# Performance work log

Measured on AMD Instinct MI355X. Metric: run time of the kernel, lower is better.

Reference implementation:

```python
import jax, jax.numpy as jnp
import numpy as np

B, C_IN, H, W = 4, 1536, 64, 64   # SGI input: cat of three 512-ch encoder maps at 64x64
HID, OUT = 1536, 512
N = H * W


def _grid_edge_index(h, w):
    # 4-connected bidirectional grid, matching SGI.grid_edge_index
    idx = np.arange(h * w).reshape(h, w)
    right = np.stack([idx[:, :-1].ravel(), idx[:, 1:].ravel()])
    down = np.stack([idx[:-1, :].ravel(), idx[1:, :].ravel()])
    ei = np.concatenate([right, down, right[::-1], down[::-1]], axis=1)
    return ei.astype(np.int32)


def setup_inputs() -> dict:
    key = jax.random.key(0)
    ks = jax.random.split(key, 7)
    ei = _grid_edge_index(H, W)
    s = 0.02
    return {
        "x":  jax.random.normal(ks[0], (B, C_IN, H, W), jnp.float32),
        "W1": jax.random.normal(ks[1], (C_IN, HID), jnp.float32) * s,
        "b1": jnp.zeros((HID,), jnp.float32),
        "W2": jax.random.normal(ks[2], (HID, OUT), jnp.float32) * s,
        "b2": jnp.zeros((OUT,), jnp.float32),
        "Wl": jax.random.normal(ks[3], (C_IN, OUT), jnp.float32) * s,
        "bl": jnp.zeros((OUT,), jnp.float32),
        "src": jnp.asarray(ei[0]),
        "dst": jnp.asarray(ei[1]),
    }


def _gcn(h_in, Wt, b, src, dst, inv_sqrt_deg, inv_deg):
    # PyG GCNConv: lin -> symmetric-normalized aggregation (with self loops) -> +bias
    h = h_in @ Wt                                   # [B, N, F]
    norm = inv_sqrt_deg[src] * inv_sqrt_deg[dst]    # [E]
    msgs = h[:, src, :] * norm[None, :, None]       # [B, E, F]
    # self-loop contribution has norm 1/deg_i
    agg = (h * inv_deg[None, :, None]).at[:, dst, :].add(msgs)
    return agg + b


def reference(x, W1, b1, W2, b2, Wl, bl, src, dst):
    Bb, C, Hh, Ww = x.shape
    n = Hh * Ww
    # degree including self loop (graph is symmetric)
    deg = jnp.zeros((n,), x.dtype).at[dst].add(1.0) + 1.0
    inv_sqrt_deg = jax.lax.rsqrt(deg)
    inv_deg = 1.0 / deg

    xt = x.reshape(Bb, C, n).transpose(0, 2, 1)     # [B, N, C]
    identity = xt
    origin = xt @ Wl + bl                           # [B, N, OUT]
    h = jax.nn.relu(_gcn(xt, W1, b1, src, dst, inv_sqrt_deg, inv_deg))
    h = _gcn(h + identity, W2, b2, src, dst, inv_sqrt_deg, inv_deg)
    out = h * origin                                # [B, N, OUT]
    return out.transpose(0, 2, 1).reshape(Bb, out.shape[-1], Hh, Ww)
```

## Files before the change

kernel.cpp:

```cpp
#include <hip/hip_runtime.h>
#include <hip/hip_bf16.h>
#include <stdint.h>


typedef __bf16 bf16;
typedef float f32x4 __attribute__((ext_vector_type(4)));
typedef bf16 bf16x8 __attribute__((ext_vector_type(8)));

#define NB 4
#define NN 4096
#define CIN 1536
#define HIDF 1536
#define OUTF 512

__global__ __launch_bounds__(256) void transpose_cvt(
    const float* __restrict__ in, bf16* __restrict__ out,
    int R, int Cc, long in_bstride, long out_bstride) {
  __shared__ float tile[32][33];
  const float* inb = in + (long)blockIdx.z * in_bstride;
  bf16* outb = out + (long)blockIdx.z * out_bstride;
  const int c0 = blockIdx.x * 32, r0 = blockIdx.y * 32;
  const int tx = threadIdx.x, ty = threadIdx.y;
#pragma unroll
  for (int i = 0; i < 4; i++)
    tile[ty + i * 8][tx] = inb[(long)(r0 + ty + i * 8) * Cc + c0 + tx];
  __syncthreads();
#pragma unroll
  for (int i = 0; i < 4; i++)
    outb[(long)(c0 + ty + i * 8) * R + r0 + tx] = (bf16)tile[tx][ty + i * 8];
}

__device__ __forceinline__ void async_copy16(const void* g, void* l) {
  __builtin_amdgcn_global_load_lds(
      (const __attribute__((address_space(1))) void*)g,
      (__attribute__((address_space(3))) void*)l, 16, 0, 0);
}

template <typename OutT, bool ADD_BIAS>
__global__ __launch_bounds__(256) void gemm_bt(
    const bf16* __restrict__ A, const bf16* __restrict__ Bw,
    OutT* __restrict__ C, const float* __restrict__ bias, int Nf, int K) {
  __shared__ bf16 As[128 * 64];
  __shared__ bf16 Bs[128 * 64];
  const int t = threadIdx.x;
  const int wave = t >> 6, lane = t & 63;
  const int wm = (wave & 1) * 64, wn = (wave >> 1) * 64;
  const int m0 = blockIdx.x * 128;
  const int n0 = blockIdx.y * 128;
  const bf16* Ab = A + (long)blockIdx.z * NN * K + (long)m0 * K;
  const bf16* Bb = Bw + (long)n0 * K;
  OutT* Cb = C + (long)blockIdx.z * NN * Nf;

  const int r = lane >> 3;
  const int c8 = lane & 7;
  const int fchunk = c8 ^ r;

  f32x4 acc[4][4];
#pragma unroll
  for (int i = 0; i < 4; i++)
#pragma unroll
    for (int j = 0; j < 4; j++) acc[i][j] = {0.f, 0.f, 0.f, 0.f};

  const int quad = lane >> 4;
  const int l15 = lane & 15;

  for (int kt = 0; kt < K; kt += 64) {
#pragma unroll
    for (int i = 0; i < 4; i++) {
      const int row = i * 32 + wave * 8;
      async_copy16(Ab + (long)(row + r) * K + kt + fchunk * 8,
                   &As[row * 64]);
      async_copy16(Bb + (long)(row + r) * K + kt + fchunk * 8,
                   &Bs[row * 64]);
    }
    __syncthreads();
#pragma unroll
    for (int kk = 0; kk < 2; kk++) {
      const int q = kk * 4 + quad;
      bf16x8 af[4], bfv[4];
#pragma unroll
      for (int mr = 0; mr < 4; mr++) {
        const int m = wm + mr * 16 + l15;
        af[mr] = *(const bf16x8*)&As[m * 64 + (q ^ (m & 7)) * 8];
      }
#pragma unroll
      for (int nc = 0; nc < 4; nc++) {
        const int n = wn + nc * 16 + l15;
        bfv[nc] = *(const bf16x8*)&Bs[n * 64 + (q ^ (n & 7)) * 8];
      }
#pragma unroll
      for (int mr = 0; mr < 4; mr++)
#pragma unroll
        for (int nc = 0; nc < 4; nc++)
          acc[mr][nc] = __builtin_amdgcn_mfma_f32_16x16x32_bf16(
              af[mr], bfv[nc], acc[mr][nc], 0, 0, 0);
    }
    __syncthreads();
  }

#pragma unroll
  for (int mr = 0; mr < 4; mr++) {
#pragma unroll
    for (int nc = 0; nc < 4; nc++) {
      const int gn = n0 + wn + nc * 16 + l15;
      float bv = 0.f;
      if (ADD_BIAS) bv = bias[gn];
#pragma unroll
      for (int j = 0; j < 4; j++) {
        const int gm = m0 + wm + mr * 16 + quad * 4 + j;
        Cb[(long)gm * Nf + gn] = (OutT)(acc[mr][nc][j] + bv);
      }
    }
  }
}

__device__ __forceinline__ float degree_of(int n) {
  const int x = n & 63, y = n >> 6;
  return 1.0f + (x > 0) + (x < 63) + (y > 0) + (y < 63);
}

__global__ __launch_bounds__(192) void stencil1(
    const bf16* __restrict__ G1, const float* __restrict__ b1, bf16* xt) {
  const int n = blockIdx.x, b = blockIdx.y;
  const int t = threadIdx.x;
  const int gx = n & 63, gy = n >> 6;
  const float degn = degree_of(n);
  const float wself = 1.0f / degn;
  const long base = ((long)b * NN + n) * (long)HIDF + t * 8;

  float acc[8];
  {
    bf16x8 v = *(const bf16x8*)(G1 + base);
#pragma unroll
    for (int i = 0; i < 8; i++) acc[i] = (float)v[i] * wself;
  }
  if (gx > 0) {
    const float w = rsqrtf(degn * degree_of(n - 1));
    bf16x8 u = *(const bf16x8*)(G1 + base - HIDF);
#pragma unroll
    for (int i = 0; i < 8; i++) acc[i] += (float)u[i] * w;
  }
  if (gx < 63) {
    const float w = rsqrtf(degn * degree_of(n + 1));
    bf16x8 u = *(const bf16x8*)(G1 + base + HIDF);
#pragma unroll
    for (int i = 0; i < 8; i++) acc[i] += (float)u[i] * w;
  }
  if (gy > 0) {
    const float w = rsqrtf(degn * degree_of(n - 64));
    bf16x8 u = *(const bf16x8*)(G1 + base - 64L * HIDF);
#pragma unroll
    for (int i = 0; i < 8; i++) acc[i] += (float)u[i] * w;
  }
  if (gy < 63) {
    const float w = rsqrtf(degn * degree_of(n + 64));
    bf16x8 u = *(const bf16x8*)(G1 + base + 64L * HIDF);
#pragma unroll
    for (int i = 0; i < 8; i++) acc[i] += (float)u[i] * w;
  }

  bf16x8 xv = *(const bf16x8*)(xt + base);
  bf16x8 o;
#pragma unroll
  for (int i = 0; i < 8; i++) {
    float h = acc[i] + b1[t * 8 + i];
    h = h > 0.f ? h : 0.f;
    o[i] = (bf16)(h + (float)xv[i]);
  }
  *(bf16x8*)(xt + base) = o;
}

__global__ __launch_bounds__(256) void stencil2(
    const float* __restrict__ G2, const float* __restrict__ Orig,
    const float* __restrict__ b2, float* __restrict__ out) {
  __shared__ float tile[16][513];
  const int n0 = blockIdx.x * 16, b = blockIdx.y;
  const int t = threadIdx.x;
  const int fq = t & 127, nl = t >> 7;
  const int f = fq * 4;
  const f32x4 bv = *(const f32x4*)(b2 + f);
#pragma unroll
  for (int p = 0; p < 8; p++) {
    const int nLoc = p * 2 + nl;
    const int n = n0 + nLoc;
    const int gx = n & 63, gy = n >> 6;
    const float degn = degree_of(n);
    const float ws = 1.0f / degn;
    const long rb = ((long)b * NN + n) * (long)OUTF + f;
    f32x4 g = *(const f32x4*)(G2 + rb);
    f32x4 a;
#pragma unroll
    for (int i = 0; i < 4; i++) a[i] = g[i] * ws;
    if (gx > 0) {
      const float w = rsqrtf(degn * degree_of(n - 1));
      f32x4 u = *(const f32x4*)(G2 + rb - OUTF);
#pragma unroll
      for (int i = 0; i < 4; i++) a[i] += u[i] * w;
    }
    if (gx < 63) {
      const float w = rsqrtf(degn * degree_of(n + 1));
      f32x4 u = *(const f32x4*)(G2 + rb + OUTF);
#pragma unroll
      for (int i = 0; i < 4; i++) a[i] += u[i] * w;
    }
    if (gy > 0) {
      const float w = rsqrtf(degn * degree_of(n - 64));
      f32x4 u = *(const f32x4*)(G2 + rb - 64L * OUTF);
#pragma unroll
      for (int i = 0; i < 4; i++) a[i] += u[i] * w;
    }
    if (gy < 63) {
      const float w = rsqrtf(degn * degree_of(n + 64));
      f32x4 u = *(const f32x4*)(G2 + rb + 64L * OUTF);
#pragma unroll
      for (int i = 0; i < 4; i++) a[i] += u[i] * w;
    }
    f32x4 og = *(const f32x4*)(Orig + rb);
#pragma unroll
    for (int i = 0; i < 4; i++) tile[nLoc][f + i] = (a[i] + bv[i]) * og[i];
  }
  __syncthreads();
  const int nl2 = t & 15, f0 = t >> 4;
#pragma unroll
  for (int q = 0; q < 32; q++) {
    const int ff = q * 16 + f0;
    out[((long)b * OUTF + ff) * (long)NN + n0 + nl2] = tile[nl2][ff];
  }
}

extern "C" void kernel_launch(void* const* d_in, const int* in_sizes, int n_in,
                              void* d_out, int out_size, void* d_ws,
                              size_t ws_size, hipStream_t stream) {
  const float* x = (const float*)d_in[0];
  const float* W1 = (const float*)d_in[1];
  const float* b1 = (const float*)d_in[2];
  const float* W2 = (const float*)d_in[3];
  const float* b2 = (const float*)d_in[4];
  const float* Wl = (const float*)d_in[5];
  const float* bl = (const float*)d_in[6];
  float* out = (float*)d_out;

  uint8_t* ws = (uint8_t*)d_ws;
  size_t off = 0;
  auto alloc = [&](size_t bytes) -> void* {
    void* p = ws + off;
    off += (bytes + 255) & ~(size_t)255;
    return p;
  };
  bf16* xt = (bf16*)alloc((size_t)NB * NN * CIN * 2);
  bf16* g1 = (bf16*)alloc((size_t)NB * NN * HIDF * 2);
  bf16* w1t = (bf16*)alloc((size_t)HIDF * CIN * 2);
  bf16* w2t = (bf16*)alloc((size_t)OUTF * HIDF * 2);
  bf16* wlt = (bf16*)alloc((size_t)OUTF * CIN * 2);
  float* g2 = (float*)alloc((size_t)NB * NN * OUTF * 4);
  float* origin = (float*)alloc((size_t)NB * NN * OUTF * 4);

  const dim3 tb(32, 8);
  transpose_cvt<<<dim3(NN / 32, CIN / 32, NB), tb, 0, stream>>>(
      x, xt, CIN, NN, (long)CIN * NN, (long)NN * CIN);
  transpose_cvt<<<dim3(HIDF / 32, CIN / 32, 1), tb, 0, stream>>>(
      W1, w1t, CIN, HIDF, 0, 0);
  transpose_cvt<<<dim3(OUTF / 32, HIDF / 32, 1), tb, 0, stream>>>(
      W2, w2t, HIDF, OUTF, 0, 0);
  transpose_cvt<<<dim3(OUTF / 32, CIN / 32, 1), tb, 0, stream>>>(
      Wl, wlt, CIN, OUTF, 0, 0);

  gemm_bt<bf16, false><<<dim3(NN / 128, HIDF / 128, NB), 256, 0, stream>>>(
      xt, w1t, g1, nullptr, HIDF, CIN);
  gemm_bt<float, true><<<dim3(NN / 128, OUTF / 128, NB), 256, 0, stream>>>(
      xt, wlt, origin, bl, OUTF, CIN);
  stencil1<<<dim3(NN, NB), 192, 0, stream>>>(g1, b1, xt);
  gemm_bt<float, false><<<dim3(NN / 128, OUTF / 128, NB), 256, 0, stream>>>(
      xt, w2t, g2, nullptr, OUTF, HIDF);
  stencil2<<<dim3(NN / 16, NB), 256, 0, stream>>>(g2, origin, b2, out);
}
```

Measured before the change: 399.4 us.

## Merge transposes and the two input GEMMs into single launches, remap stencil blocks

Folds the four transpose/convert launches into one prep kernel and concatenates W1 and Wl so the first GEMM and the origin GEMM run as one launch over a wider N dimension. Stencil1 now handles 8 nodes per block and reads its bias once, and both stencil kernels permute their block index so that consecutive blocks land on spread-out node ranges. The aim is to cut launch count, tail effects and bias reloads. It adds index arithmetic and may reduce L2 locality for the neighbour reads in the stencils.

```diff
diff --git a/kernel.cpp b/kernel.cpp
--- a/kernel.cpp
+++ b/kernel.cpp
@@ -13,21 +13,50 @@
 #define HIDF 1536
 #define OUTF 512
 
-__global__ __launch_bounds__(256) void transpose_cvt(
-    const float* __restrict__ in, bf16* __restrict__ out,
-    int R, int Cc, long in_bstride, long out_bstride) {
+__device__ __forceinline__ void tcvt(const float* __restrict__ in,
+                                     bf16* __restrict__ out, int R, int Cc,
+                                     int c0, int r0, int t,
+                                     float (*tile)[33]) {
+  const int tx = t & 31, ty = t >> 5;
+#pragma unroll
+  for (int i = 0; i < 4; i++)
+    tile[ty + i * 8][tx] = in[(long)(r0 + ty + i * 8) * Cc + c0 + tx];
+  __syncthreads();
+#pragma unroll
+  for (int i = 0; i < 4; i++)
+    out[(long)(c0 + ty + i * 8) * R + r0 + tx] = (bf16)tile[tx][ty + i * 8];
+}
+
+#define XTILES (NB * (NN / 32) * (CIN / 32))
+#define W1TILES ((CIN / 32) * (HIDF / 32))
+#define W2TILES ((HIDF / 32) * (OUTF / 32))
+#define WLTILES ((CIN / 32) * (OUTF / 32))
+
+__global__ __launch_bounds__(256) void prep(
+    const float* __restrict__ x, const float* __restrict__ W1,
+    const float* __restrict__ W2, const float* __restrict__ Wl,
+    bf16* __restrict__ xt, bf16* __restrict__ w1t, bf16* __restrict__ w2t,
+    bf16* __restrict__ wlt) {
   __shared__ float tile[32][33];
-  const float* inb = in + (long)blockIdx.z * in_bstride;
-  bf16* outb = out + (long)blockIdx.z * out_bstride;
-  const int c0 = blockIdx.x * 32, r0 = blockIdx.y * 32;
-  const int tx = threadIdx.x, ty = threadIdx.y;
-#pragma unroll
-  for (int i = 0; i < 4; i++)
-    tile[ty + i * 8][tx] = inb[(long)(r0 + ty + i * 8) * Cc + c0 + tx];
-  __syncthreads();
-#pragma unroll
-  for (int i = 0; i < 4; i++)
-    outb[(long)(c0 + ty + i * 8) * R + r0 + tx] = (bf16)tile[tx][ty + i * 8];
+  const int b = blockIdx.x, t = threadIdx.x;
+  if (b < XTILES) {
+    const int batch = b / (XTILES / NB), local = b % (XTILES / NB);
+    const int cx = local & 127, ry = local >> 7;
+    tcvt(x + (long)batch * CIN * NN, xt + (long)batch * NN * CIN, CIN, NN,
+         cx * 32, ry * 32, t, tile);
+  } else if (b < XTILES + W1TILES) {
+    const int local = b - XTILES;
+    const int cx = local % 48, ry = local / 48;
+    tcvt(W1, w1t, CIN, HIDF, cx * 32, ry * 32, t, tile);
+  } else if (b < XTILES + W1TILES + W2TILES) {
+    const int local = b - XTILES - W1TILES;
+    const int cx = local % 16, ry = local / 16;
+    tcvt(W2, w2t, HIDF, OUTF, cx * 32, ry * 32, t, tile);
+  } else {
+    const int local = b - XTILES - W1TILES - W2TILES;
+    const int cx = local % 16, ry = local / 16;
+    tcvt(Wl, wlt, CIN, OUTF, cx * 32, ry * 32, t, tile);
+  }
 }
 
 __device__ __forceinline__ void async_copy16(const void* g, void* l) {
@@ -36,82 +65,126 @@
       (__attribute__((address_space(3))) void*)l, 16, 0, 0);
 }
 
-template <typename OutT, bool ADD_BIAS>
-__global__ __launch_bounds__(256) void gemm_bt(
+struct GemmCtx {
+  f32x4 acc[4][4];
+  int wave, lane, wm, wn, quad, l15;
+};
+
+template <int K>
+__device__ __forceinline__ void gemm_kloop(GemmCtx& cx, const bf16* Ab,
+                                           const bf16* Bb, bf16* As,
+                                           bf16* Bs) {
+  const int r = cx.lane >> 3, c8 = cx.lane & 7;
+  const int fchunk = c8 ^ r;
+  for (int kt = 0; kt < K; kt += 64) {
+#pragma unroll
+    for (int i = 0; i < 4; i++) {
+      const int row = i * 32 + cx.wave * 8;
+      async_copy16(Ab + (long)(row + r) * K + kt + fchunk * 8, &As[row * 64]);
+      async_copy16(Bb + (long)(row + r) * K + kt + fchunk * 8, &Bs[row * 64]);
+    }
+    __syncthreads();
+#pragma unroll
+    for (int kk = 0; kk < 2; kk++) {
+      const int q = kk * 4 + cx.quad;
+      bf16x8 af[4], bfv[4];
+#pragma unroll
+      for (int mr = 0; mr < 4; mr++) {
+        const int m = cx.wm + mr * 16 + cx.l15;
+        af[mr] = *(const bf16x8*)&As[m * 64 + (q ^ (m & 7)) * 8];
+      }
+#pragma unroll
+      for (int nc = 0; nc < 4; nc++) {
+        const int n = cx.wn + nc * 16 + cx.l15;
+        bfv[nc] = *(const bf16x8*)&Bs[n * 64 + (q ^ (n & 7)) * 8];
+      }
+#pragma unroll
+      for (int mr = 0; mr < 4; mr++)
+#pragma unroll
+        for (int nc = 0; nc < 4; nc++)
+          cx.acc[mr][nc] = __builtin_amdgcn_mfma_f32_16x16x32_bf16(
+              af[mr], bfv[nc], cx.acc[mr][nc], 0, 0, 0);
+    }
+    __syncthreads();
+  }
+}
+
+__device__ __forceinline__ void gemm_init(GemmCtx& cx, int t) {
+  cx.wave = t >> 6;
+  cx.lane = t & 63;
+  cx.wm = (cx.wave & 1) * 64;
+  cx.wn = (cx.wave >> 1) * 64;
+  cx.quad = cx.lane >> 4;
+  cx.l15 = cx.lane & 15;
+#pragma unroll
+  for (int i = 0; i < 4; i++)
+#pragma unroll
+    for (int j = 0; j < 4; j++) cx.acc[i][j] = {0.f, 0.f, 0.f, 0.f};
+}
+
+__global__ __launch_bounds__(256) void gemm_dual(
     const bf16* __restrict__ A, const bf16* __restrict__ Bw,
-    OutT* __restrict__ C, const float* __restrict__ bias, int Nf, int K) {
+    bf16* __restrict__ G1, float* __restrict__ Orig,
+    const float* __restrict__ bl) {
   __shared__ bf16 As[128 * 64];
   __shared__ bf16 Bs[128 * 64];
-  const int t = threadIdx.x;
-  const int wave = t >> 6, lane = t & 63;
-  const int wm = (wave & 1) * 64, wn = (wave >> 1) * 64;
-  const int m0 = blockIdx.x * 128;
-  const int n0 = blockIdx.y * 128;
-  const bf16* Ab = A + (long)blockIdx.z * NN * K + (long)m0 * K;
-  const bf16* Bb = Bw + (long)n0 * K;
-  OutT* Cb = C + (long)blockIdx.z * NN * Nf;
-
-  const int r = lane >> 3;
-  const int c8 = lane & 7;
-  const int fchunk = c8 ^ r;
-
-  f32x4 acc[4][4];
-#pragma unroll
-  for (int i = 0; i < 4; i++)
-#pragma unroll
-    for (int j = 0; j < 4; j++) acc[i][j] = {0.f, 0.f, 0.f, 0.f};
-
-  const int quad = lane >> 4;
-  const int l15 = lane & 15;
-
-  for (int kt = 0; kt < K; kt += 64) {
-#pragma unroll
-    for (int i = 0; i < 4; i++) {
-      const int row = i * 32 + wave * 8;
-      async_copy16(Ab + (long)(row + r) * K + kt + fchunk * 8,
-                   &As[row * 64]);
-      async_copy16(Bb + (long)(row + r) * K + kt + fchunk * 8,
-                   &Bs[row * 64]);
-    }
-    __syncthreads();
-#pragma unroll
-    for (int kk = 0; kk < 2; kk++) {
-      const int q = kk * 4 + quad;
-      bf16x8 af[4], bfv[4];
-#pragma unroll
-      for (int mr = 0; mr < 4; mr++) {
-        const int m = wm + mr * 16 + l15;
-        af[mr] = *(const bf16x8*)&As[m * 64 + (q ^ (m & 7)) * 8];
-      }
+  GemmCtx cx;
+  gemm_init(cx, threadIdx.x);
+  const int m0 = blockIdx.x * 128, n0 = blockIdx.y * 128, z = blockIdx.z;
+  gemm_kloop<CIN>(cx, A + (long)z * NN * CIN + (long)m0 * CIN,
+                  Bw + (long)n0 * CIN, As, Bs);
+  if (n0 < HIDF) {
+    bf16* Cb = G1 + (long)z * NN * HIDF;
+#pragma unroll
+    for (int mr = 0; mr < 4; mr++)
 #pragma unroll
       for (int nc = 0; nc < 4; nc++) {
-        const int n = wn + nc * 16 + l15;
-        bfv[nc] = *(const bf16x8*)&Bs[n * 64 + (q ^ (n & 7)) * 8];
-      }
-#pragma unroll
-      for (int mr = 0; mr < 4; mr++)
-#pragma unroll
-        for (int nc = 0; nc < 4; nc++)
-          acc[mr][nc] = __builtin_amdgcn_mfma_f32_16x16x32_bf16(
-              af[mr], bfv[nc], acc[mr][nc], 0, 0, 0);
-    }
-    __syncthreads();
-  }
-
-#pragma unroll
-  for (int mr = 0; mr < 4; mr++) {
+        const int gn = n0 + cx.wn + nc * 16 + cx.l15;
+#pragma unroll
+        for (int j = 0; j < 4; j++) {
+          const int gm = m0 + cx.wm + mr * 16 + cx.quad * 4 + j;
+          Cb[(long)gm * HIDF + gn] = (bf16)cx.acc[mr][nc][j];
+        }
+      }
+  } else {
+    float* Cb = Orig + (long)z * NN * OUTF;
+#pragma unroll
+    for (int mr = 0; mr < 4; mr++)
+#pragma unroll
+      for (int nc = 0; nc < 4; nc++) {
+        const int gn = (n0 - HIDF) + cx.wn + nc * 16 + cx.l15;
+        const float bv = bl[gn];
+#pragma unroll
+        for (int j = 0; j < 4; j++) {
+          const int gm = m0 + cx.wm + mr * 16 + cx.quad * 4 + j;
+          Cb[(long)gm * OUTF + gn] = cx.acc[mr][nc][j] + bv;
+        }
+      }
+  }
+}
+
+__global__ __launch_bounds__(256) void gemm_f32(
+    const bf16* __restrict__ A, const bf16* __restrict__ Bw,
+    float* __restrict__ C, int Nf) {
+  __shared__ bf16 As[128 * 64];
+  __shared__ bf16 Bs[128 * 64];
+  GemmCtx cx;
+  gemm_init(cx, threadIdx.x);
+  const int m0 = blockIdx.x * 128, n0 = blockIdx.y * 128, z = blockIdx.z;
+  gemm_kloop<HIDF>(cx, A + (long)z * NN * HIDF + (long)m0 * HIDF,
+                   Bw + (long)n0 * HIDF, As, Bs);
+  float* Cb = C + (long)z * NN * Nf;
+#pragma unroll
+  for (int mr = 0; mr < 4; mr++)
 #pragma unroll
     for (int nc = 0; nc < 4; nc++) {
-      const int gn = n0 + wn + nc * 16 + l15;
-      float bv = 0.f;
-      if (ADD_BIAS) bv = bias[gn];
+      const int gn = n0 + cx.wn + nc * 16 + cx.l15;
 #pragma unroll
       for (int j = 0; j < 4; j++) {
-        const int gm = m0 + wm + mr * 16 + quad * 4 + j;
-        Cb[(long)gm * Nf + gn] = (OutT)(acc[mr][nc][j] + bv);
-      }
-    }
-  }
+        const int gm = m0 + cx.wm + mr * 16 + cx.quad * 4 + j;
+        Cb[(long)gm * Nf + gn] = cx.acc[mr][nc][j];
+      }
+    }
 }
 
 __device__ __forceinline__ float degree_of(int n) {
@@ -121,60 +194,72 @@
 
 __global__ __launch_bounds__(192) void stencil1(
     const bf16* __restrict__ G1, const float* __restrict__ b1, bf16* xt) {
-  const int n = blockIdx.x, b = blockIdx.y;
-  const int t = threadIdx.x;
-  const int gx = n & 63, gy = n >> 6;
-  const float degn = degree_of(n);
-  const float wself = 1.0f / degn;
-  const long base = ((long)b * NN + n) * (long)HIDF + t * 8;
-
-  float acc[8];
+  const int blk = blockIdx.x;
+  const int s = ((blk & 7) << 6) + (blk >> 3);
+  const int b = blockIdx.y, t = threadIdx.x;
+  float bias[8];
   {
-    bf16x8 v = *(const bf16x8*)(G1 + base);
-#pragma unroll
-    for (int i = 0; i < 8; i++) acc[i] = (float)v[i] * wself;
-  }
-  if (gx > 0) {
-    const float w = rsqrtf(degn * degree_of(n - 1));
-    bf16x8 u = *(const bf16x8*)(G1 + base - HIDF);
-#pragma unroll
-    for (int i = 0; i < 8; i++) acc[i] += (float)u[i] * w;
-  }
-  if (gx < 63) {
-    const float w = rsqrtf(degn * degree_of(n + 1));
-    bf16x8 u = *(const bf16x8*)(G1 + base + HIDF);
-#pragma unroll
-    for (int i = 0; i < 8; i++) acc[i] += (float)u[i] * w;
-  }
-  if (gy > 0) {
-    const float w = rsqrtf(degn * degree_of(n - 64));
-    bf16x8 u = *(const bf16x8*)(G1 + base - 64L * HIDF);
-#pragma unroll
-    for (int i = 0; i < 8; i++) acc[i] += (float)u[i] * w;
-  }
-  if (gy < 63) {
-    const float w = rsqrtf(degn * degree_of(n + 64));
-    bf16x8 u = *(const bf16x8*)(G1 + base + 64L * HIDF);
-#pragma unroll
-    for (int i = 0; i < 8; i++) acc[i] += (float)u[i] * w;
-  }
-
-  bf16x8 xv = *(const bf16x8*)(xt + base);
-  bf16x8 o;
-#pragma unroll
-  for (int i = 0; i < 8; i++) {
-    float h = acc[i] + b1[t * 8 + i];
-    h = h > 0.f ? h : 0.f;
-    o[i] = (bf16)(h + (float)xv[i]);
-  }
-  *(bf16x8*)(xt + base) = o;
+    f32x4 b0 = *(const f32x4*)(b1 + t * 8);
+    f32x4 b4 = *(const f32x4*)(b1 + t * 8 + 4);
+#pragma unroll
+    for (int i = 0; i < 4; i++) { bias[i] = b0[i]; bias[4 + i] = b4[i]; }
+  }
+#pragma unroll 1
+  for (int p = 0; p < 8; p++) {
+    const int n = s * 8 + p;
+    const int gx = n & 63, gy = n >> 6;
+    const float degn = degree_of(n);
+    const float wself = 1.0f / degn;
+    const long base = ((long)b * NN + n) * (long)HIDF + t * 8;
+    float acc[8];
+    {
+      bf16x8 v = *(const bf16x8*)(G1 + base);
+#pragma unroll
+      for (int i = 0; i < 8; i++) acc[i] = (float)v[i] * wself;
+    }
+    if (gx > 0) {
+      const float w = rsqrtf(degn * degree_of(n - 1));
+      bf16x8 u = *(const bf16x8*)(G1 + base - HIDF);
+#pragma unroll
+      for (int i = 0; i < 8; i++) acc[i] += (float)u[i] * w;
+    }
+    if (gx < 63) {
+      const float w = rsqrtf(degn * degree_of(n + 1));
+      bf16x8 u = *(const bf16x8*)(G1 + base + HIDF);
+#pragma unroll
+      for (int i = 0; i < 8; i++) acc[i] += (float)u[i] * w;
+    }
+    if (gy > 0) {
+      const float w = rsqrtf(degn * degree_of(n - 64));
+      bf16x8 u = *(const bf16x8*)(G1 + base - 64L * HIDF);
+#pragma unroll
+      for (int i = 0; i < 8; i++) acc[i] += (float)u[i] * w;
+    }
+    if (gy < 63) {
+      const float w = rsqrtf(degn * degree_of(n + 64));
+      bf16x8 u = *(const bf16x8*)(G1 + base + 64L * HIDF);
+#pragma unroll
+      for (int i = 0; i < 8; i++) acc[i] += (float)u[i] * w;
+    }
+    bf16x8 xv = *(const bf16x8*)(xt + base);
+    bf16x8 o;
+#pragma unroll
+    for (int i = 0; i < 8; i++) {
+      float h = acc[i] + bias[i];
+      h = h > 0.f ? h : 0.f;
+      o[i] = (bf16)(h + (float)xv[i]);
+    }
+    *(bf16x8*)(xt + base) = o;
+  }
 }
 
 __global__ __launch_bounds__(256) void stencil2(
     const float* __restrict__ G2, const float* __restrict__ Orig,
     const float* __restrict__ b2, float* __restrict__ out) {
   __shared__ float tile[16][513];
-  const int n0 = blockIdx.x * 16, b = blockIdx.y;
+  const int blk = blockIdx.x;
+  const int s = ((blk & 7) << 5) + (blk >> 3);
+  const int n0 = s * 16, b = blockIdx.y;
   const int t = threadIdx.x;
   const int fq = t & 127, nl = t >> 7;
   const int f = fq * 4;
@@ -249,28 +334,23 @@
   };
   bf16* xt = (bf16*)alloc((size_t)NB * NN * CIN * 2);
   bf16* g1 = (bf16*)alloc((size_t)NB * NN * HIDF * 2);
-  bf16* w1t = (bf16*)alloc((size_t)HIDF * CIN * 2);
+  bf16* wcat = (bf16*)alloc((size_t)(HIDF + OUTF) * CIN * 2);
+  bf16* w1t = wcat;
+  bf16* wlt = wcat + (size_t)HIDF * CIN;
   bf16* w2t = (bf16*)alloc((size_t)OUTF * HIDF * 2);
-  bf16* wlt = (bf16*)alloc((size_t)OUTF * CIN * 2);
   float* g2 = (float*)alloc((size_t)NB * NN * OUTF * 4);
   float* origin = (float*)alloc((size_t)NB * NN * OUTF * 4);
 
-  const dim3 tb(32, 8);
-  transpose_cvt<<<dim3(NN / 32, CIN / 32, NB), tb, 0, stream>>>(
-      x, xt, CIN, NN, (long)CIN * NN, (long)NN * CIN);
-  transpose_cvt<<<dim3(HIDF / 32, CIN / 32, 1), tb, 0, stream>>>(
-      W1, w1t, CIN, HIDF, 0, 0);
-  transpose_cvt<<<dim3(OUTF / 32, HIDF / 32, 1), tb, 0, stream>>>(
-      W2, w2t, HIDF, OUTF, 0, 0);
-  transpose_cvt<<<dim3(OUTF / 32, CIN / 32, 1), tb, 0, stream>>>(
-      Wl, wlt, CIN, OUTF, 0, 0);
-
-  gemm_bt<bf16, false><<<dim3(NN / 128, HIDF / 128, NB), 256, 0, stream>>>(
-      xt, w1t, g1, nullptr, HIDF, CIN);
-  gemm_bt<float, true><<<dim3(NN / 128, OUTF / 128, NB), 256, 0, stream>>>(
-      xt, wlt, origin, bl, OUTF, CIN);
-  stencil1<<<dim3(NN, NB), 192, 0, stream>>>(g1, b1, xt);
-  gemm_bt<float, false><<<dim3(NN / 128, OUTF / 128, NB), 256, 0, stream>>>(
-      xt, w2t, g2, nullptr, OUTF, HIDF);
-  stencil2<<<dim3(NN / 16, NB), 256, 0, stream>>>(g2, origin, b2, out);
-}
+  prep<<<XTILES + W1TILES + W2TILES + WLTILES, 256, 0, stream>>>(
+      x, W1, W2, Wl, xt, w1t, w2t, wlt);
+
+  gemm_dual<<<dim3(NN / 128, (HIDF + OUTF) / 128, NB), 256, 0, stream>>>(
+      xt, wcat, g1, origin, bl);
+
+  stencil1<<<dim3(512, NB), 192, 0, stream>>>(g1, b1, xt);
+
+  gemm_f32<<<dim3(NN / 128, OUTF / 128, NB), 256, 0, stream>>>(xt, w2t, g2,
+                                                               OUTF);
+
+  stencil2<<<dim3(256, NB), 256, 0, stream>>>(g2, origin, b2, out);
+}
```

New measurement: 394.3 us. No clear change (-1.3%).
